# Kernel tuning notes

Hardware: AMD Instinct MI355X
Metric: run time of the kernel (lower is better)

Reference implementation:

```python
import jax, jax.numpy as jnp
import numpy as np

B, L, HID, NH = 1, 2048, 3072, 24
HD = HID // NH          # 128
MLP = HID * 4           # 12288


def _layernorm(x, eps=1e-6):
    # LayerNorm without affine (pre_norm)
    mu = jnp.mean(x, axis=-1, keepdims=True)
    var = jnp.mean(jnp.square(x - mu), axis=-1, keepdims=True)
    return (x - mu) * jax.lax.rsqrt(var + eps)


def _rmsnorm(x, w):
    # torch.nn.RMSNorm with eps=None -> finfo(dtype).eps
    eps = jnp.finfo(x.dtype).eps
    ms = jnp.mean(jnp.square(x), axis=-1, keepdims=True)
    return x * jax.lax.rsqrt(ms + eps) * w


def _apply_rope(x, pe):
    # x: (B, L, H, D); pe: (B, 1, L, D//2, 2, 2)
    b, l, h, d = x.shape
    x_ = x.astype(jnp.float32).reshape(b, l, h, d // 2, 1, 2)
    f = pe[:, :, :, None]                       # (B,1,L,1,D//2,2,2)
    out = f[..., 0] * x_[..., 0] + f[..., 1] * x_[..., 1]
    return out.reshape(b, l, h, d).astype(x.dtype)


def setup_inputs() -> dict:
    key = jax.random.key(0)
    ks = jax.random.split(key, 16)
    s = 0.02
    # pe as proper 2x2 rotation matrices (EmbedND output structure)
    theta = jax.random.uniform(ks[0], (L, HD // 2), minval=0.0, maxval=2.0 * np.pi)
    cos, sin = jnp.cos(theta), jnp.sin(theta)
    rot = jnp.stack([jnp.stack([cos, -sin], -1), jnp.stack([sin, cos], -1)], -2)
    pe = rot[None, None].astype(jnp.float32)    # (1,1,L,HD//2,2,2)
    rnd = lambda k, shp: jax.random.normal(k, shp, jnp.float32)
    return {
        "x": rnd(ks[1], (B, L, HID)),
        "vec": rnd(ks[2], (B, HID)),
        "pe": pe,
        "w_mod": rnd(ks[3], (HID, 3 * HID)) * s,
        "b_mod": rnd(ks[4], (3 * HID,)) * s,
        "w_qkv": rnd(ks[5], (HID, 3 * HID)) * s,
        "b_qkv": rnd(ks[6], (3 * HID,)) * s,
        "w_fc1": rnd(ks[7], (HID, MLP)) * s,
        "b_fc1": rnd(ks[8], (MLP,)) * s,
        "w_fc2": rnd(ks[9], (MLP, HID)) * s,
        "b_fc2": rnd(ks[10], (HID,)) * s,
        "w_out": rnd(ks[11], (HID, HID)) * s,
        "b_out": rnd(ks[12], (HID,)) * s,
        "norm_q_w": jnp.ones((HD,), jnp.float32),
        "norm_k_w": jnp.ones((HD,), jnp.float32),
    }


def reference(x, vec, pe, w_mod, b_mod, w_qkv, b_qkv, w_fc1, b_fc1,
              w_fc2, b_fc2, w_out, b_out, norm_q_w, norm_k_w):
    # modulation: AWQ linear on silu(vec)
    mod = jax.nn.silu(vec) @ w_mod + b_mod            # (B, 3*HID)
    shift, scale, gate = jnp.split(mod[:, None, :], 3, axis=-1)
    x_mod = _layernorm(x) * (1.0 + scale) + shift      # (B, L, HID)

    # qkv projection (SVDQ linear, dequantized math == dense GEMM)
    qkv = x_mod @ w_qkv + b_qkv
    q, k, v = jnp.split(qkv, 3, axis=-1)
    q = _rmsnorm(q.reshape(B, L, NH, HD), norm_q_w)
    k = _rmsnorm(k.reshape(B, L, NH, HD), norm_k_w)
    q = _apply_rope(q, pe)
    k = _apply_rope(k, pe)
    v = v.reshape(B, L, NH, HD)

    # scaled dot-product attention
    scores = jnp.einsum("blhd,bmhd->bhlm", q, k) / jnp.sqrt(jnp.float32(HD))
    probs = jax.nn.softmax(scores, axis=-1)
    attn = jnp.einsum("bhlm,bmhd->blhd", probs, v).reshape(B, L, HID)

    # parallel MLP branch
    mlp = jax.nn.gelu(x_mod @ w_fc1 + b_fc1, approximate=True)
    mlp = mlp @ w_fc2 + b_fc2

    out = attn @ w_out + b_out + mlp
    return x + gate * out
```

## Files before the change

kernel.cpp:

```cpp
#include <hip/hip_runtime.h>
#include <hip/hip_bf16.h>
#include <stdint.h>


typedef __bf16 bf16;
typedef bf16 bf16x2 __attribute__((ext_vector_type(2)));
typedef bf16 bf16x4 __attribute__((ext_vector_type(4)));
typedef bf16 bf16x8 __attribute__((ext_vector_type(8)));
typedef float f32x4 __attribute__((ext_vector_type(4)));

#define L_SEQ 2048
#define HIDD  3072
#define NHH   24
#define HDD   128
#define MLPD  12288
#define N3Q   9216

struct PB { bf16* p[8]; };

__device__ __forceinline__ void gload_lds16(const bf16* g, bf16* l) {
  __builtin_amdgcn_global_load_lds(
      (const __attribute__((address_space(1))) unsigned int*)g,
      (__attribute__((address_space(3))) unsigned int*)l, 16, 0, 0);
}

__device__ __forceinline__ float gelu_tanh(float x) {
  float z = 0.7978845608028654f * (x + 0.044715f * x * x * x);
  float t = 1.f - 2.f / (__expf(2.f * z) + 1.f);
  return 0.5f * x * (1.f + t);
}

__global__ __launch_bounds__(256) void mod_partial(
    const float* __restrict__ vec, const float* __restrict__ w_mod,
    float* __restrict__ part) {
  __shared__ float sv[256];
  int y = blockIdx.y;
  int i0 = y * 256;
  {
    float xv = vec[i0 + threadIdx.x];
    sv[threadIdx.x] = xv / (1.f + __expf(-xv));
  }
  __syncthreads();
  int j = blockIdx.x * 256 + threadIdx.x;
  float acc = 0.f;
#pragma unroll 8
  for (int i = 0; i < 256; ++i)
    acc += sv[i] * w_mod[(size_t)(i0 + i) * N3Q + j];
  part[y * N3Q + j] = acc;
}

__global__ __launch_bounds__(256) void mod_reduce(
    const float* __restrict__ part, const float* __restrict__ b_mod,
    float* __restrict__ mod) {
  int j = blockIdx.x * 256 + threadIdx.x;
  float s = b_mod[j];
#pragma unroll
  for (int p = 0; p < 12; ++p) s += part[p * N3Q + j];
  mod[j] = s;
}

__global__ __launch_bounds__(256) void ln_mod_k(
    const float* __restrict__ x, const float* __restrict__ mod,
    bf16* __restrict__ xm) {
  __shared__ float sb[4];
  int l = blockIdx.x, t = threadIdx.x;
  const float* xr = x + (size_t)l * HIDD;
  float4 v[3];
  float s = 0.f;
#pragma unroll
  for (int p = 0; p < 3; ++p) {
    v[p] = *(const float4*)(xr + p * 1024 + t * 4);
    s += v[p].x + v[p].y + v[p].z + v[p].w;
  }
#pragma unroll
  for (int o = 32; o >= 1; o >>= 1) s += __shfl_xor(s, o);
  if (!(t & 63)) sb[t >> 6] = s;
  __syncthreads();
  float mean = (sb[0] + sb[1] + sb[2] + sb[3]) * (1.f / HIDD);
  __syncthreads();
  float vs = 0.f;
#pragma unroll
  for (int p = 0; p < 3; ++p) {
    float a = v[p].x - mean, b = v[p].y - mean, c = v[p].z - mean,
          d = v[p].w - mean;
    vs += a * a + b * b + c * c + d * d;
  }
#pragma unroll
  for (int o = 32; o >= 1; o >>= 1) vs += __shfl_xor(vs, o);
  if (!(t & 63)) sb[t >> 6] = vs;
  __syncthreads();
  float var = (sb[0] + sb[1] + sb[2] + sb[3]) * (1.f / HIDD);
  float rs = rsqrtf(var + 1e-6f);
#pragma unroll
  for (int p = 0; p < 3; ++p) {
    int j = p * 1024 + t * 4;
    float4 sc = *(const float4*)(mod + HIDD + j);
    float4 sh = *(const float4*)(mod + j);
    bf16x4 o;
    o[0] = (bf16)((v[p].x - mean) * rs * (1.f + sc.x) + sh.x);
    o[1] = (bf16)((v[p].y - mean) * rs * (1.f + sc.y) + sh.y);
    o[2] = (bf16)((v[p].z - mean) * rs * (1.f + sc.z) + sh.z);
    o[3] = (bf16)((v[p].w - mean) * rs * (1.f + sc.w) + sh.w);
    *(bf16x4*)(xm + (size_t)l * HIDD + j) = o;
  }
}

__global__ __launch_bounds__(256) void convT(
    const float* __restrict__ src, bf16* __restrict__ dst, int K, int N) {
  __shared__ bf16 tl[64 * 72];
  int n0 = blockIdx.x * 64, k0 = blockIdx.y * 64;
  int t = threadIdx.x;
#pragma unroll
  for (int p = 0; p < 4; ++p) {
    int idx = p * 256 + t;
    int kr = idx >> 4, c4 = (idx & 15) << 2;
    float4 v = *(const float4*)(src + (size_t)(k0 + kr) * N + n0 + c4);
    bf16x4 b;
    b[0] = (bf16)v.x; b[1] = (bf16)v.y; b[2] = (bf16)v.z; b[3] = (bf16)v.w;
    *(bf16x4*)(tl + kr * 72 + c4) = b;
  }
  __syncthreads();
#pragma unroll
  for (int p = 0; p < 2; ++p) {
    int idx = p * 256 + t;
    int nr = idx >> 3, c = idx & 7;
    bf16x8 o;
#pragma unroll
    for (int j = 0; j < 8; ++j) o[j] = tl[(c * 8 + j) * 72 + nr];
    *(bf16x8*)(dst + (size_t)(n0 + nr) * K + k0 + c * 8) = o;
  }
}

template <int EPI>
__global__ __launch_bounds__(512, 2) void gemm256(
    const bf16* __restrict__ A, const bf16* __restrict__ BT,
    const float* __restrict__ bias, int lda, int klen, int ldc, int gy,
    int gz, PB dst, const bf16* __restrict__ BT2,
    const bf16* __restrict__ BT3) {
  __shared__ bf16 LA[2][2][8192];
  __shared__ bf16 LB[2][2][8192];
  const int tid = threadIdx.x;
  const int w = tid >> 6, lane = tid & 63;
  const int wm = w >> 2, wn = w & 3;
  const int g = lane >> 4, r16 = lane & 15;
  const int hb = wn >> 1, brow = (wn & 1) * 64;

  const int nwg = 8 * gy * gz;
  int id = (int)blockIdx.x;
  int sw = (id & 7) * (nwg >> 3) + (id >> 3);
  const int bx = sw & 7;
  const int rem = sw >> 3;
  const int by = rem % gy;
  const int bz = rem / gy;

  const int row0 = bx * 256, col0 = by * 256;
  const size_t kb = (size_t)bz * klen;

  const int s_r = tid >> 3, s_c = tid & 7;
  const bf16* gA = A + (size_t)(row0 + s_r) * lda + kb + ((s_c ^ (s_r & 7)) << 3);
  const bf16* bbase = BT;
  int bcol = col0;
  if (EPI == 2) {
    if (by >= 36)      { bbase = BT3; bcol = col0 - 9216; }
    else if (by >= 32) { bbase = BT2; bcol = col0 - 8192; }
  }
  const bf16* gB =
      bbase + (size_t)(bcol + s_r) * lda + kb + ((s_c ^ (s_r & 7)) << 3);
  const int wofs = w * 512;

#define STG_A(buf, h, t)                                                       \
  do {                                                                         \
    gload_lds16(gA + (size_t)((h) * 128) * lda + (size_t)(t) * 64,             \
                &LA[buf][h][wofs]);                                            \
    gload_lds16(gA + (size_t)((h) * 128 + 64) * lda + (size_t)(t) * 64,        \
                &LA[buf][h][4096 + wofs]);                                     \
  } while (0)
#define STG_B(buf, h, t)                                                       \
  do {                                                                         \
    gload_lds16(gB + (size_t)((h) * 128) * lda + (size_t)(t) * 64,             \
                &LB[buf][h][wofs]);                                            \
    gload_lds16(gB + (size_t)((h) * 128 + 64) * lda + (size_t)(t) * 64,        \
                &LB[buf][h][4096 + wofs]);                                     \
  } while (0)
#define LGKM0()                                               \
  do {                                                        \
    asm volatile("s_waitcnt lgkmcnt(0)" ::: "memory");        \
    __builtin_amdgcn_sched_barrier(0);                        \
  } while (0)
#define RD_A4(DST, LAP, MB)                                                    \
  _Pragma("unroll") for (int m_ = 0; m_ < 4; ++m_)                             \
  _Pragma("unroll") for (int kk_ = 0; kk_ < 2; ++kk_)                          \
      DST[m_][kk_] = *(const bf16x8*)((LAP) + (((MB) + m_) * 16 + r16) * 64 +  \
                                      (((kk_ * 4 + g) ^ (r16 & 7)) << 3));
#define RD_B2(DST, LBP, NB)                                                    \
  _Pragma("unroll") for (int n_ = 0; n_ < 2; ++n_)                             \
  _Pragma("unroll") for (int kk_ = 0; kk_ < 2; ++kk_)                          \
      DST[n_][kk_] = *(const bf16x8*)(                                         \
          (LBP) + (brow + ((NB) + n_) * 16 + r16) * 64 +                       \
          (((kk_ * 4 + g) ^ (r16 & 7)) << 3));
#define QUAD(AF, BF, MB, NB)                                                   \
  do {                                                                         \
    __builtin_amdgcn_s_setprio(1);                                             \
    _Pragma("unroll") for (int kk_ = 0; kk_ < 2; ++kk_)                        \
    _Pragma("unroll") for (int m_ = 0; m_ < 4; ++m_)                           \
    _Pragma("unroll") for (int n_ = 0; n_ < 2; ++n_)                           \
        acc[(MB) + m_][(NB) + n_] = __builtin_amdgcn_mfma_f32_16x16x32_bf16(   \
            AF[m_][kk_], BF[n_][kk_], acc[(MB) + m_][(NB) + n_], 0, 0, 0);     \
    __builtin_amdgcn_s_setprio(0);                                             \
  } while (0)

#define GROUP(TB, T1, T2)                                                      \
  do {                                                                         \
    const bf16* la = &LA[TB][wm][0];                                           \
    const bf16* lb = &LB[TB][hb][0];                                           \
    bf16x8 aL[4][2], aH[4][2], bL[2][2], bH[2][2];                             \
                                           \
    RD_A4(aL, la, 0);                                                          \
    RD_B2(bL, lb, 0);                                                          \
    if ((T1) < nk) STG_B(TB ^ 1, 1, T1);                                       \
    asm volatile("s_waitcnt lgkmcnt(8)" ::: "memory");                         \
    __builtin_amdgcn_s_barrier();                                              \
    LGKM0();                                                                   \
    QUAD(aL, bL, 0, 0);                                                        \
    __builtin_amdgcn_s_barrier();                                              \
                      \
    RD_A4(aH, la, 4);                                                          \
    __builtin_amdgcn_s_barrier();                                              \
    LGKM0();                                                                   \
    QUAD(aH, bL, 4, 0);                                                        \
    __builtin_amdgcn_s_barrier();                                              \
     \
    RD_B2(bH, lb, 2);                                                          \
    if ((T2) < nk) { STG_A(TB, 0, T2); STG_A(TB, 1, T2); }                     \
    __builtin_amdgcn_s_barrier();                                              \
    LGKM0();                                                                   \
    QUAD(aL, bH, 0, 2);                                                        \
    __builtin_amdgcn_s_barrier();                                              \
       \
    if ((T2) < nk) {                                                           \
      STG_B(TB, 0, T2);                                                        \
      asm volatile("s_waitcnt vmcnt(6)" ::: "memory");                         \
    } else {                                                                   \
      asm volatile("s_waitcnt vmcnt(0)" ::: "memory");                         \
    }                                                                          \
    __builtin_amdgcn_s_barrier();                                              \
    QUAD(aH, bH, 4, 2);                                                        \
    __builtin_amdgcn_s_barrier();                                              \
  } while (0)

  f32x4 acc[8][4] = {};
  const int nk = klen >> 6;

  STG_A(0, 0, 0); STG_A(0, 1, 0); STG_B(0, 0, 0); STG_B(0, 1, 0);
  STG_A(1, 0, 1); STG_A(1, 1, 1); STG_B(1, 0, 1);
  asm volatile("s_waitcnt vmcnt(6)" ::: "memory");
  __builtin_amdgcn_s_barrier();

  for (int t = 0; t < nk; t += 2) {
    GROUP(0, t + 1, t + 2);
    GROUP(1, t + 2, t + 3);
  }
#undef STG_A
#undef STG_B
#undef LGKM0
#undef RD_A4
#undef RD_B2
#undef QUAD
#undef GROUP

  if (EPI == 2 && by < 36) {
    bf16* dp = dst.p[0];
#pragma unroll
    for (int m = 0; m < 8; ++m) {
      int row = row0 + wm * 128 + m * 16 + g * 4;
#pragma unroll
      for (int n = 0; n < 4; ++n) {
        int col = col0 + wn * 64 + n * 16 + r16;
#pragma unroll
        for (int r = 0; r < 4; ++r)
          dp[(size_t)(row + r) * N3Q + col] = (bf16)acc[m][n][r];
      }
    }
  } else if (EPI == 2) {
    bf16* dp = dst.p[1];
#pragma unroll
    for (int m = 0; m < 8; ++m) {
      int row = row0 + wm * 128 + m * 16 + g * 4;
#pragma unroll
      for (int n = 0; n < 4; ++n) {
        int col = col0 - 9216 + wn * 64 + n * 16 + r16;
        float bv = bias[col];
#pragma unroll
        for (int r = 0; r < 4; ++r)
          dp[(size_t)(row + r) * MLPD + col] = (bf16)gelu_tanh(acc[m][n][r] + bv);
      }
    }
  } else {
    bf16* dp = dst.p[bz];
#pragma unroll
    for (int m = 0; m < 8; ++m) {
      int row = row0 + wm * 128 + m * 16 + g * 4;
#pragma unroll
      for (int n = 0; n < 4; ++n) {
        int col = col0 + wn * 64 + n * 16 + r16;
#pragma unroll
        for (int r = 0; r < 4; ++r)
          dp[(size_t)(row + r) * ldc + col] = (bf16)acc[m][n][r];
      }
    }
  }
}

__global__ __launch_bounds__(256) void qknorm_rope_k(
    const bf16* __restrict__ P, const float* __restrict__ b_qkv,
    const float* __restrict__ pe, const float* __restrict__ qw,
    const float* __restrict__ kw, bf16* __restrict__ qb,
    bf16* __restrict__ kb) {
  int t = threadIdx.x, lane = t & 63, w = t >> 6;
  int pair = blockIdx.x * 4 + w;
  int h = pair % NHH, l = pair / NHH;
  size_t qi = (size_t)l * N3Q + h * HDD + 2 * lane;
  size_t ob = (size_t)l * HIDD + h * HDD + 2 * lane;
  float4 f = *(const float4*)(pe + (size_t)l * 256 + lane * 4);
  float2 wq = *(const float2*)(qw + 2 * lane);
  float2 wk = *(const float2*)(kw + 2 * lane);
  {
    bf16x2 a = *(const bf16x2*)(P + qi);
    float2 bq = *(const float2*)(b_qkv + h * HDD + 2 * lane);
    float x0 = (float)a[0] + bq.x;
    float x1 = (float)a[1] + bq.y;
    float ss = x0 * x0 + x1 * x1;
#pragma unroll
    for (int o = 32; o >= 1; o >>= 1) ss += __shfl_xor(ss, o);
    float rs = rsqrtf(ss * (1.f / HDD) + 1.1920929e-7f);
    x0 *= rs * wq.x; x1 *= rs * wq.y;
    const float qs = 0.08838834764831845f;
    bf16x2 ov;
    ov[0] = (bf16)((f.x * x0 + f.y * x1) * qs);
    ov[1] = (bf16)((f.z * x0 + f.w * x1) * qs);
    *(bf16x2*)(qb + ob) = ov;
  }
  {
    bf16x2 a = *(const bf16x2*)(P + qi + HIDD);
    float2 bk = *(const float2*)(b_qkv + HIDD + h * HDD + 2 * lane);
    float x0 = (float)a[0] + bk.x;
    float x1 = (float)a[1] + bk.y;
    float ss = x0 * x0 + x1 * x1;
#pragma unroll
    for (int o = 32; o >= 1; o >>= 1) ss += __shfl_xor(ss, o);
    float rs = rsqrtf(ss * (1.f / HDD) + 1.1920929e-7f);
    x0 *= rs * wk.x; x1 *= rs * wk.y;
    bf16x2 ov;
    ov[0] = (bf16)(f.x * x0 + f.y * x1);
    ov[1] = (bf16)(f.z * x0 + f.w * x1);
    *(bf16x2*)(kb + ob) = ov;
  }
}

__global__ __launch_bounds__(256) void vtrans_k(
    const bf16* __restrict__ P, const float* __restrict__ b_qkv,
    bf16* __restrict__ vt) {
  __shared__ bf16 tl[128 * 128];
  int t = threadIdx.x, lt = blockIdx.x, h = blockIdx.y;
#pragma unroll
  for (int p = 0; p < 8; ++p) {
    int idx = p * 256 + t;
    int i = idx >> 4, c = idx & 15;
    size_t gi = (size_t)(lt * 128 + i) * N3Q + 2 * HIDD + h * HDD + c * 8;
    bf16x8 a = *(const bf16x8*)(P + gi);
    bf16x8 val;
#pragma unroll
    for (int e = 0; e < 8; ++e)
      val[e] = (bf16)((float)a[e] + b_qkv[2 * HIDD + h * HDD + c * 8 + e]);
    *(bf16x8*)(tl + i * 128 + ((c ^ (i & 15)) << 3)) = val;
  }
  __syncthreads();
#pragma unroll
  for (int p = 0; p < 8; ++p) {
    int idx = p * 256 + t;
    int j = idx >> 4, i8 = (idx & 15) << 3;
    bf16x8 o;
#pragma unroll
    for (int e = 0; e < 8; ++e) {
      int row = i8 + e;
      o[e] = tl[row * 128 + ((((j >> 3) ^ (row & 15)) << 3) | (j & 7))];
    }
    *(bf16x8*)(vt + ((size_t)h * HDD + j) * L_SEQ + lt * 128 + i8) = o;
  }
}

__global__ __launch_bounds__(256) void attn_k(
    const bf16* __restrict__ q, const bf16* __restrict__ k,
    const bf16* __restrict__ vt, bf16* __restrict__ out) {
  __shared__ bf16 Ks[64 * 128];
  __shared__ bf16 Vs[128 * 64];
  __shared__ bf16 Ps[4][16 * 72];
  int tid = threadIdx.x, lane = tid & 63, w = tid >> 6;
  int g = lane >> 4, r16 = lane & 15;
  int qt = blockIdx.x, h = blockIdx.y;
  int qbase = qt * 64 + w * 16;

  bf16x8 qreg[4];
  const bf16* qrow = q + (size_t)(qbase + r16) * HIDD + h * HDD;
#pragma unroll
  for (int c = 0; c < 4; ++c) qreg[c] = *(const bf16x8*)(qrow + c * 32 + g * 8);

  f32x4 acc[8] = {};
  float m_run = -3.0e38f, l_run = 0.f;
  bf16* ps = &Ps[w][0];

  for (int kv0 = 0; kv0 < L_SEQ; kv0 += 64) {
    __syncthreads();
#pragma unroll
    for (int p = 0; p < 4; ++p) {
      int ci = p * 256 + tid;
      {
        int rr = ci >> 4, cc = ci & 15;
        gload_lds16(k + (size_t)(kv0 + rr) * HIDD + h * HDD +
                        ((cc ^ (rr & 15)) << 3),
                    Ks + ((p * 4 + w) << 9));
      }
      {
        int rr = ci >> 3, cc = ci & 7;
        gload_lds16(vt + ((size_t)h * HDD + rr) * L_SEQ + kv0 +
                        ((cc ^ (rr & 7)) << 3),
                    Vs + ((p * 4 + w) << 9));
      }
    }
    __syncthreads();

    f32x4 st[4] = {};
#pragma unroll
    for (int m4 = 0; m4 < 4; ++m4) {
#pragma unroll
      for (int c = 0; c < 4; ++c) {
        int rr = m4 * 16 + r16;
        bf16x8 kf =
            *(const bf16x8*)(Ks + rr * 128 + (((c * 4 + g) ^ (rr & 15)) << 3));
        st[m4] =
            __builtin_amdgcn_mfma_f32_16x16x32_bf16(kf, qreg[c], st[m4], 0, 0, 0);
      }
    }
    float cmax = -3.0e38f;
#pragma unroll
    for (int m4 = 0; m4 < 4; ++m4)
#pragma unroll
      for (int r = 0; r < 4; ++r) cmax = fmaxf(cmax, st[m4][r]);
    cmax = fmaxf(cmax, __shfl_xor(cmax, 16));
    cmax = fmaxf(cmax, __shfl_xor(cmax, 32));
    float m_new = fmaxf(m_run, cmax);
    float corr = __expf(m_run - m_new);
    float psum = 0.f;
#pragma unroll
    for (int m4 = 0; m4 < 4; ++m4) {
      bf16x4 pk;
#pragma unroll
      for (int r = 0; r < 4; ++r) {
        float pv = __expf(st[m4][r] - m_new);
        psum += pv;
        pk[r] = (bf16)pv;
      }
      *(bf16x4*)(ps + r16 * 72 + m4 * 16 + g * 4) = pk;
    }
    psum += __shfl_xor(psum, 16);
    psum += __shfl_xor(psum, 32);
    l_run = l_run * corr + psum;
    m_run = m_new;
    float corr_r[4];
#pragma unroll
    for (int r = 0; r < 4; ++r) corr_r[r] = __shfl(corr, g * 4 + r);
#pragma unroll
    for (int nt = 0; nt < 8; ++nt)
#pragma unroll
      for (int r = 0; r < 4; ++r) acc[nt][r] *= corr_r[r];
#pragma unroll
    for (int ks = 0; ks < 2; ++ks) {
      bf16x8 pf = *(const bf16x8*)(ps + r16 * 72 + ks * 32 + g * 8);
#pragma unroll
      for (int nt = 0; nt < 8; ++nt) {
        int rr = nt * 16 + r16;
        bf16x8 vf =
            *(const bf16x8*)(Vs + rr * 64 + (((ks * 4 + g) ^ (rr & 7)) << 3));
        acc[nt] = __builtin_amdgcn_mfma_f32_16x16x32_bf16(pf, vf, acc[nt], 0, 0, 0);
      }
    }
  }
  float inv = 1.f / l_run;
  float inv_r[4];
#pragma unroll
  for (int r = 0; r < 4; ++r) inv_r[r] = __shfl(inv, g * 4 + r);
#pragma unroll
  for (int nt = 0; nt < 8; ++nt)
#pragma unroll
    for (int r = 0; r < 4; ++r)
      out[(size_t)(qbase + g * 4 + r) * HIDD + h * HDD + nt * 16 + r16] =
          (bf16)(acc[nt][r] * inv_r[r]);
}

__global__ __launch_bounds__(256) void osum_k(
    const bf16* __restrict__ a, const bf16* __restrict__ b,
    const bf16* __restrict__ c, const bf16* __restrict__ d,
    float* __restrict__ o) {
  size_t i = ((size_t)blockIdx.x * 256 + threadIdx.x) * 4;
  bf16x4 va = *(const bf16x4*)(a + i);
  bf16x4 vb = *(const bf16x4*)(b + i);
  bf16x4 vc = *(const bf16x4*)(c + i);
  bf16x4 vd = *(const bf16x4*)(d + i);
  float4 s;
  s.x = (float)va[0] + (float)vb[0] + (float)vc[0] + (float)vd[0];
  s.y = (float)va[1] + (float)vb[1] + (float)vc[1] + (float)vd[1];
  s.z = (float)va[2] + (float)vb[2] + (float)vc[2] + (float)vd[2];
  s.w = (float)va[3] + (float)vb[3] + (float)vc[3] + (float)vd[3];
  *(float4*)(o + i) = s;
}

__global__ __launch_bounds__(256) void final_k(
    const float* __restrict__ x, PB ps, const float* __restrict__ mod,
    const float* __restrict__ b_out, const float* __restrict__ b_fc2,
    float* __restrict__ out) {
  int l = blockIdx.x, t = threadIdx.x;
#pragma unroll
  for (int p = 0; p < 3; ++p) {
    int c = p * 1024 + t * 4;
    size_t idx = (size_t)l * HIDD + c;
    float4 xv = *(const float4*)(x + idx);
    float4 gv = *(const float4*)(mod + 2 * HIDD + c);
    float4 bo = *(const float4*)(b_out + c);
    float4 bf = *(const float4*)(b_fc2 + c);
    float4 da = *(const float4*)(out + idx);
    float a0 = da.x + bo.x + bf.x, a1 = da.y + bo.y + bf.y;
    float a2 = da.z + bo.z + bf.z, a3 = da.w + bo.w + bf.w;
#pragma unroll
    for (int i = 0; i < 8; ++i) {
      bf16x4 v = *(const bf16x4*)(ps.p[i] + idx);
      a0 += (float)v[0]; a1 += (float)v[1];
      a2 += (float)v[2]; a3 += (float)v[3];
    }
    float4 o;
    o.x = xv.x + gv.x * a0;
    o.y = xv.y + gv.y * a1;
    o.z = xv.z + gv.z * a2;
    o.w = xv.w + gv.w * a3;
    *(float4*)(out + idx) = o;
  }
}

extern "C" void kernel_launch(void* const* d_in, const int* in_sizes, int n_in,
                              void* d_out, int out_size, void* d_ws,
                              size_t ws_size, hipStream_t stream) {
  const float* x     = (const float*)d_in[0];
  const float* vec   = (const float*)d_in[1];
  const float* pe    = (const float*)d_in[2];
  const float* w_mod = (const float*)d_in[3];
  const float* b_mod = (const float*)d_in[4];
  const float* w_qkv = (const float*)d_in[5];
  const float* b_qkv = (const float*)d_in[6];
  const float* w_fc1 = (const float*)d_in[7];
  const float* b_fc1 = (const float*)d_in[8];
  const float* w_fc2 = (const float*)d_in[9];
  const float* b_fc2 = (const float*)d_in[10];
  const float* w_out = (const float*)d_in[11];
  const float* b_out = (const float*)d_in[12];
  const float* qw    = (const float*)d_in[13];
  const float* kw    = (const float*)d_in[14];
  float* out = (float*)d_out;

  char* ws = (char*)d_ws;
  float* mod  = (float*)(ws + 0);
  bf16* xmod  = (bf16*)(ws + 65536);
  bf16* qb    = (bf16*)(ws + 12648448);
  bf16* kbuf  = (bf16*)(ws + 25231360);
  bf16* vt    = (bf16*)(ws + 37814272);
  bf16* att   = (bf16*)(ws + 50397184);
  bf16* mlpF  = (bf16*)(ws + 62980096);
  bf16* wt    = (bf16*)(ws + 113311744);
  bf16* P0    = (bf16*)(ws + 188809216);
  float* part = (float*)(ws + 188809216);
  bf16* H1    = (bf16*)(ws + 188809216 + 12582912);
  bf16* H2    = (bf16*)(ws + 188809216 + 25165824);
  bf16* wtQlo = qb;
  bf16* wtScr = (bf16*)out;
  PB Z = {};

  mod_partial<<<dim3(36, 12), 256, 0, stream>>>(vec, w_mod, part);
  mod_reduce<<<36, 256, 0, stream>>>(part, b_mod, mod);
  ln_mod_k<<<2048, 256, 0, stream>>>(x, mod, xmod);

  convT<<<dim3(128, 48), 256, 0, stream>>>(w_qkv, wtQlo, 3072, 9216);
  convT<<<dim3(16, 48), 256, 0, stream>>>(w_qkv + 8192, wtScr, 3072, 9216);
  convT<<<dim3(192, 48), 256, 0, stream>>>(w_fc1, wt, 3072, 12288);
  PB Pc = {}; Pc.p[0] = P0; Pc.p[1] = mlpF;
  gemm256<2><<<672, 512, 0, stream>>>(xmod, wtQlo, b_fc1, 3072, 3072, 0, 84,
                                      1, Pc, wtScr, wt);

  qknorm_rope_k<<<12288, 256, 0, stream>>>(P0, b_qkv, pe, qw, kw, qb, kbuf);
  vtrans_k<<<dim3(16, 24), 256, 0, stream>>>(P0, b_qkv, vt);
  attn_k<<<dim3(32, 24), 256, 0, stream>>>(qb, kbuf, vt, att);

  convT<<<dim3(48, 48), 256, 0, stream>>>(w_out, wt, 3072, 3072);
  PB Po = {}; Po.p[0] = qb; Po.p[1] = kbuf; Po.p[2] = vt; Po.p[3] = P0;
  gemm256<0><<<384, 512, 0, stream>>>(att, wt, nullptr, 3072, 768, 3072, 12, 4,
                                      Po, nullptr, nullptr);
  osum_k<<<6144, 256, 0, stream>>>(qb, kbuf, vt, P0, out);

  convT<<<dim3(48, 192), 256, 0, stream>>>(w_fc2, wt, 12288, 3072);
  PB Pf = {};
  Pf.p[0] = xmod; Pf.p[1] = qb; Pf.p[2] = kbuf; Pf.p[3] = vt;
  Pf.p[4] = att;  Pf.p[5] = P0; Pf.p[6] = H1;   Pf.p[7] = H2;
  gemm256<0><<<768, 512, 0, stream>>>(mlpF, wt, nullptr, 12288, 1536, 3072, 12,
                                      8, Pf, nullptr, nullptr);

  final_k<<<2048, 256, 0, stream>>>(x, Pf, mod, b_out, b_fc2, out);
}
```

Before: 848.7 us.

## Fuse out-projection and fc2 GEMMs into one split-K launch with fp32 slice

Merges the attention output projection and the MLP fc2 projection into a single GEMM launch (EPI 3). Slice 0 computes att@w_out over its full K and writes fp32 straight into the output buffer. Four further slices split fc2's K=12288 into 3072-wide chunks written as bf16 partials. This removes the separate out-proj launch, the osum_k reduction pass and four extra partial buffers, so final_k sums fewer partials. It also reshapes split-K from 8x1536 to 4x3072, which changes grid size and per-block K length and could affect load balance.

Result: faster. 812.1 us (-4.3%).

```diff
diff --git a/kernel.cpp b/kernel.cpp
--- a/kernel.cpp
+++ b/kernel.cpp
@@ -16,7 +16,7 @@
 #define MLPD  12288
 #define N3Q   9216
 
-struct PB { bf16* p[8]; };
+struct PB { bf16* p[4]; };
 
 __device__ __forceinline__ void gload_lds16(const bf16* g, bf16* l) {
   __builtin_amdgcn_global_load_lds(
@@ -134,9 +134,9 @@
 template <int EPI>
 __global__ __launch_bounds__(512, 2) void gemm256(
     const bf16* __restrict__ A, const bf16* __restrict__ BT,
-    const float* __restrict__ bias, int lda, int klen, int ldc, int gy,
-    int gz, PB dst, const bf16* __restrict__ BT2,
-    const bf16* __restrict__ BT3) {
+    const float* __restrict__ bias, int lda, int klen, int gy, int gz,
+    PB dst, bf16* __restrict__ o1, const bf16* __restrict__ BT2,
+    const bf16* __restrict__ BT3, float* __restrict__ o32) {
   __shared__ bf16 LA[2][2][8192];
   __shared__ bf16 LB[2][2][8192];
   const int tid = threadIdx.x;
@@ -154,32 +154,42 @@
   const int bz = rem / gy;
 
   const int row0 = bx * 256, col0 = by * 256;
-  const size_t kb = (size_t)bz * klen;
 
   const int s_r = tid >> 3, s_c = tid & 7;
-  const bf16* gA = A + (size_t)(row0 + s_r) * lda + kb + ((s_c ^ (s_r & 7)) << 3);
-  const bf16* bbase = BT;
+  const int swzoff = (s_c ^ (s_r & 7)) << 3;
+
+  int lda_eff = lda;
+  const bf16* Abase = A;
+  const bf16* Bbase = BT;
+  size_t kb2 = 0;
   int bcol = col0;
   if (EPI == 2) {
-    if (by >= 36)      { bbase = BT3; bcol = col0 - 9216; }
-    else if (by >= 32) { bbase = BT2; bcol = col0 - 8192; }
-  }
-  const bf16* gB =
-      bbase + (size_t)(bcol + s_r) * lda + kb + ((s_c ^ (s_r & 7)) << 3);
+    if (by >= 36)      { Bbase = BT3; bcol = col0 - 9216; }
+    else if (by >= 32) { Bbase = BT2; bcol = col0 - 8192; }
+  } else if (EPI == 3) {
+    if (bz != 0) {
+      lda_eff = MLPD;
+      Abase = BT3;
+      Bbase = BT2;
+      kb2 = (size_t)(bz - 1) * 3072;
+    }
+  }
+  const bf16* gA = Abase + (size_t)(row0 + s_r) * lda_eff + kb2 + swzoff;
+  const bf16* gB = Bbase + (size_t)(bcol + s_r) * lda_eff + kb2 + swzoff;
   const int wofs = w * 512;
 
 #define STG_A(buf, h, t)                                                       \
   do {                                                                         \
-    gload_lds16(gA + (size_t)((h) * 128) * lda + (size_t)(t) * 64,             \
+    gload_lds16(gA + (size_t)((h) * 128) * lda_eff + (size_t)(t) * 64,         \
                 &LA[buf][h][wofs]);                                            \
-    gload_lds16(gA + (size_t)((h) * 128 + 64) * lda + (size_t)(t) * 64,        \
+    gload_lds16(gA + (size_t)((h) * 128 + 64) * lda_eff + (size_t)(t) * 64,    \
                 &LA[buf][h][4096 + wofs]);                                     \
   } while (0)
 #define STG_B(buf, h, t)                                                       \
   do {                                                                         \
-    gload_lds16(gB + (size_t)((h) * 128) * lda + (size_t)(t) * 64,             \
+    gload_lds16(gB + (size_t)((h) * 128) * lda_eff + (size_t)(t) * 64,         \
                 &LB[buf][h][wofs]);                                            \
-    gload_lds16(gB + (size_t)((h) * 128 + 64) * lda + (size_t)(t) * 64,        \
+    gload_lds16(gB + (size_t)((h) * 128 + 64) * lda_eff + (size_t)(t) * 64,    \
                 &LB[buf][h][4096 + wofs]);                                     \
   } while (0)
 #define LGKM0()                                               \
@@ -282,7 +292,7 @@
       }
     }
   } else if (EPI == 2) {
-    bf16* dp = dst.p[1];
+    bf16* dp = o1;
 #pragma unroll
     for (int m = 0; m < 8; ++m) {
       int row = row0 + wm * 128 + m * 16 + g * 4;
@@ -295,8 +305,7 @@
           dp[(size_t)(row + r) * MLPD + col] = (bf16)gelu_tanh(acc[m][n][r] + bv);
       }
     }
-  } else {
-    bf16* dp = dst.p[bz];
+  } else if (EPI == 3 && bz == 0) {
 #pragma unroll
     for (int m = 0; m < 8; ++m) {
       int row = row0 + wm * 128 + m * 16 + g * 4;
@@ -305,7 +314,20 @@
         int col = col0 + wn * 64 + n * 16 + r16;
 #pragma unroll
         for (int r = 0; r < 4; ++r)
-          dp[(size_t)(row + r) * ldc + col] = (bf16)acc[m][n][r];
+          o32[(size_t)(row + r) * HIDD + col] = acc[m][n][r];
+      }
+    }
+  } else {
+    bf16* dp = dst.p[bz - 1];
+#pragma unroll
+    for (int m = 0; m < 8; ++m) {
+      int row = row0 + wm * 128 + m * 16 + g * 4;
+#pragma unroll
+      for (int n = 0; n < 4; ++n) {
+        int col = col0 + wn * 64 + n * 16 + r16;
+#pragma unroll
+        for (int r = 0; r < 4; ++r)
+          dp[(size_t)(row + r) * HIDD + col] = (bf16)acc[m][n][r];
       }
     }
   }
@@ -497,23 +519,6 @@
           (bf16)(acc[nt][r] * inv_r[r]);
 }
 
-__global__ __launch_bounds__(256) void osum_k(
-    const bf16* __restrict__ a, const bf16* __restrict__ b,
-    const bf16* __restrict__ c, const bf16* __restrict__ d,
-    float* __restrict__ o) {
-  size_t i = ((size_t)blockIdx.x * 256 + threadIdx.x) * 4;
-  bf16x4 va = *(const bf16x4*)(a + i);
-  bf16x4 vb = *(const bf16x4*)(b + i);
-  bf16x4 vc = *(const bf16x4*)(c + i);
-  bf16x4 vd = *(const bf16x4*)(d + i);
-  float4 s;
-  s.x = (float)va[0] + (float)vb[0] + (float)vc[0] + (float)vd[0];
-  s.y = (float)va[1] + (float)vb[1] + (float)vc[1] + (float)vd[1];
-  s.z = (float)va[2] + (float)vb[2] + (float)vc[2] + (float)vd[2];
-  s.w = (float)va[3] + (float)vb[3] + (float)vc[3] + (float)vd[3];
-  *(float4*)(o + i) = s;
-}
-
 __global__ __launch_bounds__(256) void final_k(
     const float* __restrict__ x, PB ps, const float* __restrict__ mod,
     const float* __restrict__ b_out, const float* __restrict__ b_fc2,
@@ -531,7 +536,7 @@
     float a0 = da.x + bo.x + bf.x, a1 = da.y + bo.y + bf.y;
     float a2 = da.z + bo.z + bf.z, a3 = da.w + bo.w + bf.w;
 #pragma unroll
-    for (int i = 0; i < 8; ++i) {
+    for (int i = 0; i < 4; ++i) {
       bf16x4 v = *(const bf16x4*)(ps.p[i] + idx);
       a0 += (float)v[0]; a1 += (float)v[1];
       a2 += (float)v[2]; a3 += (float)v[3];
@@ -576,11 +581,9 @@
   bf16* wt    = (bf16*)(ws + 113311744);
   bf16* P0    = (bf16*)(ws + 188809216);
   float* part = (float*)(ws + 188809216);
-  bf16* H1    = (bf16*)(ws + 188809216 + 12582912);
-  bf16* H2    = (bf16*)(ws + 188809216 + 25165824);
   bf16* wtQlo = qb;
   bf16* wtScr = (bf16*)out;
-  PB Z = {};
+  bf16* wtO   = P0;
 
   mod_partial<<<dim3(36, 12), 256, 0, stream>>>(vec, w_mod, part);
   mod_reduce<<<36, 256, 0, stream>>>(part, b_mod, mod);
@@ -589,26 +592,20 @@
   convT<<<dim3(128, 48), 256, 0, stream>>>(w_qkv, wtQlo, 3072, 9216);
   convT<<<dim3(16, 48), 256, 0, stream>>>(w_qkv + 8192, wtScr, 3072, 9216);
   convT<<<dim3(192, 48), 256, 0, stream>>>(w_fc1, wt, 3072, 12288);
-  PB Pc = {}; Pc.p[0] = P0; Pc.p[1] = mlpF;
-  gemm256<2><<<672, 512, 0, stream>>>(xmod, wtQlo, b_fc1, 3072, 3072, 0, 84,
-                                      1, Pc, wtScr, wt);
+  PB Pc = {}; Pc.p[0] = P0;
+  gemm256<2><<<672, 512, 0, stream>>>(xmod, wtQlo, b_fc1, 3072, 3072, 84, 1,
+                                      Pc, mlpF, wtScr, wt, nullptr);
 
   qknorm_rope_k<<<12288, 256, 0, stream>>>(P0, b_qkv, pe, qw, kw, qb, kbuf);
   vtrans_k<<<dim3(16, 24), 256, 0, stream>>>(P0, b_qkv, vt);
   attn_k<<<dim3(32, 24), 256, 0, stream>>>(qb, kbuf, vt, att);
 
-  convT<<<dim3(48, 48), 256, 0, stream>>>(w_out, wt, 3072, 3072);
-  PB Po = {}; Po.p[0] = qb; Po.p[1] = kbuf; Po.p[2] = vt; Po.p[3] = P0;
-  gemm256<0><<<384, 512, 0, stream>>>(att, wt, nullptr, 3072, 768, 3072, 12, 4,
-                                      Po, nullptr, nullptr);
-  osum_k<<<6144, 256, 0, stream>>>(qb, kbuf, vt, P0, out);
-
+  convT<<<dim3(48, 48), 256, 0, stream>>>(w_out, wtO, 3072, 3072);
   convT<<<dim3(48, 192), 256, 0, stream>>>(w_fc2, wt, 12288, 3072);
   PB Pf = {};
   Pf.p[0] = xmod; Pf.p[1] = qb; Pf.p[2] = kbuf; Pf.p[3] = vt;
-  Pf.p[4] = att;  Pf.p[5] = P0; Pf.p[6] = H1;   Pf.p[7] = H2;
-  gemm256<0><<<768, 512, 0, stream>>>(mlpF, wt, nullptr, 12288, 1536, 3072, 12,
-                                      8, Pf, nullptr, nullptr);
+  gemm256<3><<<480, 512, 0, stream>>>(att, wtO, nullptr, 3072, 3072, 12, 5,
+                                      Pf, nullptr, wt, mlpF, out);
 
   final_k<<<2048, 256, 0, stream>>>(x, Pf, mod, b_out, b_fc2, out);
 }
```
